# Performance work log

Measured on AMD Instinct MI355X. Metric: run time of the kernel, lower is better.

## Reference

```python
import jax, jax.numpy as jnp
import numpy as np
import math

HIDDEN = 2048
NUM_HEADS = 16
NUM_KV_HEADS = 4
HEAD_DIM = HIDDEN // NUM_HEADS  # 128
INTER = 8192
ROPE_THETA = 10000.0
EPS = 1e-6
B, S = 1, 2048


def _linear_init(key, out_f, in_f):
    return jax.random.normal(key, (out_f, in_f), dtype=jnp.float32) * (2.0 / (in_f + out_f)) ** 0.5


def setup_inputs() -> dict:
    key = jax.random.key(0)
    ks = jax.random.split(key, 10)
    hidden_states = jax.random.normal(ks[0], (B, S, HIDDEN), dtype=jnp.float32)
    # additive causal mask [B, 1, S, S]
    causal = jnp.tril(jnp.ones((S, S), dtype=bool))
    attention_mask = jnp.where(causal, 0.0, -1e9).astype(jnp.float32)[None, None]
    position_ids = jnp.arange(S, dtype=jnp.int32)[None, :]
    return {
        "hidden_states": hidden_states,
        "attention_mask": attention_mask,
        "position_ids": position_ids,
        "norm1_w": jnp.ones((HIDDEN,), dtype=jnp.float32),
        "norm2_w": jnp.ones((HIDDEN,), dtype=jnp.float32),
        "Wq": _linear_init(ks[1], NUM_HEADS * HEAD_DIM, HIDDEN),
        "Wk": _linear_init(ks[2], NUM_KV_HEADS * HEAD_DIM, HIDDEN),
        "Wv": _linear_init(ks[3], NUM_KV_HEADS * HEAD_DIM, HIDDEN),
        "Wo": _linear_init(ks[4], HIDDEN, NUM_HEADS * HEAD_DIM),
        "Wgate": _linear_init(ks[5], INTER, HIDDEN),
        "Wup": _linear_init(ks[6], INTER, HIDDEN),
        "Wdown": _linear_init(ks[7], HIDDEN, INTER),
    }


def _rmsnorm(x, w):
    return x * jax.lax.rsqrt(jnp.mean(x * x, axis=-1, keepdims=True) + EPS) * w


def _apply_rope(x, position_ids):
    # x: [B, H, S, D]; split-half RoPE exactly as the torch module does
    half = x.shape[-1] // 2
    inv_freq = (1.0 / (ROPE_THETA ** (jnp.arange(0, HEAD_DIM, 2, dtype=jnp.float32) / HEAD_DIM)))[:half]
    freqs = jnp.einsum('bi,j->bij', position_ids.astype(jnp.float32), inv_freq)  # [B,S,half]
    cos = jnp.cos(freqs)[:, None]  # [B,1,S,half]
    sin = jnp.sin(freqs)[:, None]
    x1, x2 = x[..., :half], x[..., half:]
    return jnp.concatenate([x1 * cos - x2 * sin, x2 * cos + x1 * sin], axis=-1)


def reference(hidden_states, attention_mask, position_ids, norm1_w, norm2_w,
              Wq, Wk, Wv, Wo, Wgate, Wup, Wdown):
    b, s, _ = hidden_states.shape
    # --- attention sub-block (pre-norm residual) ---
    h = _rmsnorm(hidden_states, norm1_w)
    q = (h @ Wq.T).reshape(b, s, NUM_HEADS, HEAD_DIM).transpose(0, 2, 1, 3)
    k = (h @ Wk.T).reshape(b, s, NUM_KV_HEADS, HEAD_DIM).transpose(0, 2, 1, 3)
    v = (h @ Wv.T).reshape(b, s, NUM_KV_HEADS, HEAD_DIM).transpose(0, 2, 1, 3)
    q = _apply_rope(q, position_ids)
    k = _apply_rope(k, position_ids)
    n_rep = NUM_HEADS // NUM_KV_HEADS
    k = jnp.repeat(k, n_rep, axis=1)  # GQA repeat_interleave over head dim
    v = jnp.repeat(v, n_rep, axis=1)
    scores = jnp.einsum('bhqd,bhkd->bhqk', q, k) / math.sqrt(HEAD_DIM)
    scores = scores + attention_mask
    attn = jax.nn.softmax(scores, axis=-1)
    ctx = jnp.einsum('bhqk,bhkd->bhqd', attn, v).transpose(0, 2, 1, 3).reshape(b, s, -1)
    x = hidden_states + ctx @ Wo.T
    # --- MoE sub-block: num_experts == 1 -> plain SwiGLU MLP ---
    h2 = _rmsnorm(x, norm2_w)
    mlp = (jax.nn.silu(h2 @ Wgate.T) * (h2 @ Wup.T)) @ Wdown.T
    return x + mlp
```

## Files before the change

### kernel.cpp

```cpp
#include <hip/hip_runtime.h>
#include <hip/hip_bf16.h>
#include <math.h>


#define HIDDENC 2048
#define SLEN    2048
#define NHEADS  16
#define NKV     4
#define HD      128
#define INTERC  8192

typedef __attribute__((ext_vector_type(8))) short bf16x8;
typedef __attribute__((ext_vector_type(4))) float f32x4;
typedef __hip_bfloat16 bf16;

__device__ __forceinline__ void gld_lds16(const void* g, void* l) {
    __builtin_amdgcn_global_load_lds((const __attribute__((address_space(1))) void*)g,
                                     (__attribute__((address_space(3))) void*)l, 16, 0, 0);
}

__device__ __forceinline__ unsigned short bf_bits(float x) {
    bf16 t = __float2bfloat16(x);
    return *(unsigned short*)&t;
}
__device__ __forceinline__ float bits_f(short s) {
    bf16 b = *(bf16*)&s;
    return __bfloat162float(b);
}

template <int EPI>
__global__ __launch_bounds__(256) void gemm_bt(const bf16* __restrict__ A,
                                               const bf16* __restrict__ B,
                                               void* __restrict__ Cout,
                                               const float* __restrict__ R,
                                               int M, int N, int K, int lda) {
    constexpr int BM = 128, BN = 128, BK = 64;
    __shared__ bf16 As[BM * BK];
    __shared__ bf16 Bs[BN * BK];
    const int tid  = threadIdx.x;
    const int wave = tid >> 6;
    const int lane = tid & 63;
    const int wm = wave >> 1, wn = wave & 1;
    const long m0 = (long)blockIdx.y * BM;
    const long n0 = (long)blockIdx.x * BN;
    const long kofs = (long)blockIdx.z * K;

    const int srow = wave * 8 + (lane >> 3);
    const int scol = (lane & 7) * 8;
    const bf16* Ag = A + (m0 + srow) * (long)lda + scol + kofs;
    const bf16* Bg = B + (n0 + srow) * (long)lda + scol + kofs;
    bf16* Asw = &As[(wave * 8) * BK];
    bf16* Bsw = &Bs[(wave * 8) * BK];

    f32x4 acc[4][4] = {};
    const int row = lane & 15;
    const int kq  = (lane >> 4) * 8;

    for (int k0 = 0; k0 < K; k0 += BK) {
#pragma unroll
        for (int t = 0; t < 4; t++) {
            gld_lds16(Ag + (long)(t * 32) * lda + k0, Asw + t * 32 * BK);
            gld_lds16(Bg + (long)(t * 32) * lda + k0, Bsw + t * 32 * BK);
        }
        __syncthreads();
#pragma unroll
        for (int kk = 0; kk < BK; kk += 32) {
            bf16x8 af[4], bfr[4];
#pragma unroll
            for (int i = 0; i < 4; i++)
                af[i] = *(const bf16x8*)&As[(wm * 64 + i * 16 + row) * BK + kk + kq];
#pragma unroll
            for (int j = 0; j < 4; j++)
                bfr[j] = *(const bf16x8*)&Bs[(wn * 64 + j * 16 + row) * BK + kk + kq];
#pragma unroll
            for (int i = 0; i < 4; i++)
#pragma unroll
                for (int j = 0; j < 4; j++)
                    acc[i][j] = __builtin_amdgcn_mfma_f32_16x16x32_bf16(af[i], bfr[j], acc[i][j], 0, 0, 0);
        }
        __syncthreads();
    }

    const int quad = lane >> 4;
#pragma unroll
    for (int i = 0; i < 4; i++)
#pragma unroll
        for (int j = 0; j < 4; j++)
#pragma unroll
            for (int r = 0; r < 4; r++) {
                long rr = m0 + wm * 64 + i * 16 + quad * 4 + r;
                long cc = n0 + wn * 64 + j * 16 + (lane & 15);
                float v = acc[i][j][r];
                if (EPI == 0) {
                    ((bf16*)Cout)[rr * N + cc] = __float2bfloat16(v);
                } else if (EPI == 1) {
                    ((float*)Cout)[rr * N + cc] = v + R[rr * N + cc];
                } else {
                    ((float*)Cout)[(long)blockIdx.z * M * N + rr * N + cc] = v;
                }
            }
}

__global__ __launch_bounds__(256) void rmsnorm_kernel(const float* __restrict__ x,
                                                      const float* __restrict__ w,
                                                      bf16* __restrict__ out) {
    const int row = blockIdx.x;
    const int tid = threadIdx.x;
    const float* xr = x + (long)row * HIDDENC;
    float4 a = *(const float4*)&xr[tid * 8];
    float4 b = *(const float4*)&xr[tid * 8 + 4];
    float ss = a.x*a.x + a.y*a.y + a.z*a.z + a.w*a.w + b.x*b.x + b.y*b.y + b.z*b.z + b.w*b.w;
#pragma unroll
    for (int d = 1; d < 64; d <<= 1) ss += __shfl_xor(ss, d, 64);
    __shared__ float wsum[4];
    if ((tid & 63) == 0) wsum[tid >> 6] = ss;
    __syncthreads();
    ss = wsum[0] + wsum[1] + wsum[2] + wsum[3];
    float sc = rsqrtf(ss * (1.0f / HIDDENC) + 1e-6f);
    float4 wa = *(const float4*)&w[tid * 8];
    float4 wb = *(const float4*)&w[tid * 8 + 4];
    float vals[8] = {a.x*wa.x, a.y*wa.y, a.z*wa.z, a.w*wa.w,
                     b.x*wb.x, b.y*wb.y, b.z*wb.z, b.w*wb.w};
    union { bf16x8 v; unsigned short u[8]; } pk;
#pragma unroll
    for (int e = 0; e < 8; e++) pk.u[e] = bf_bits(vals[e] * sc);
    *(bf16x8*)&out[(long)row * HIDDENC + tid * 8] = pk.v;
}

__global__ __launch_bounds__(256) void cvt_kernel(const float* __restrict__ in,
                                                  bf16* __restrict__ out, long n) {
    long idx = ((long)blockIdx.x * 256 + threadIdx.x) * 8;
    if (idx >= n) return;
    float4 a = *(const float4*)&in[idx];
    float4 b = *(const float4*)&in[idx + 4];
    float vals[8] = {a.x, a.y, a.z, a.w, b.x, b.y, b.z, b.w};
    union { bf16x8 v; unsigned short u[8]; } pk;
#pragma unroll
    for (int e = 0; e < 8; e++) pk.u[e] = bf_bits(vals[e]);
    *(bf16x8*)&out[idx] = pk.v;
}

__global__ __launch_bounds__(256) void rope_kernel(bf16* __restrict__ x,
                                                   const int* __restrict__ pos,
                                                   int nheads, int rowstride) {
    long gid = (long)blockIdx.x * 256 + threadIdx.x;
    int i = gid & 63;
    long t = gid >> 6;
    int h = (int)(t % nheads);
    long s = t / nheads;
    if (s >= SLEN) return;
    float inv = __expf(-(float)i * 0.14391156516779195f);
    float f = (float)pos[s] * inv;
    float sn, c;
    sincosf(f, &sn, &c);
    bf16* p = x + s * (long)rowstride + h * HD + i;
    float x1 = __bfloat162float(p[0]);
    float x2 = __bfloat162float(p[64]);
    p[0]  = __float2bfloat16(x1 * c - x2 * sn);
    p[64] = __float2bfloat16(x2 * c + x1 * sn);
}

__global__ __launch_bounds__(256) void flash_attn(const bf16* __restrict__ Q,
                                                  const bf16* __restrict__ Kb,
                                                  const bf16* __restrict__ VT,
                                                  bf16* __restrict__ Ctx) {
    constexpr int QSTR = 2560, PSTR = 68, BKEY = 64;
    __shared__ bf16 Ks[64 * 128];
    __shared__ bf16 Vs[128 * 64];
    __shared__ bf16 Ps[4][16 * PSTR];
    const int qt  = 31 - blockIdx.x;
    const int h   = blockIdx.y;
    const int kvh = h >> 2;
    const int tid = threadIdx.x;
    const int wave = tid >> 6, lane = tid & 63;
    const int quad = lane >> 4, lrow = lane & 15;
    const int qbase = qt * 64 + wave * 16;

    bf16x8 qf[4];
#pragma unroll
    for (int kk = 0; kk < 4; kk++)
        qf[kk] = *(const bf16x8*)&Q[(long)(qbase + lrow) * QSTR + h * HD + kk * 32 + quad * 8];

    f32x4 o[8] = {};
    float mrow[4], lsum[4];
#pragma unroll
    for (int r = 0; r < 4; r++) { mrow[r] = -1e30f; lsum[r] = 0.0f; }

    const int nkt = qt + 1;
    const float scale = 0.08838834764831845f;
    const bf16* Kh  = Kb + kvh * HD;
    const bf16* VTh = VT + (long)(kvh * HD) * SLEN;
    bf16* Pw = Ps[wave];

    for (int kt = 0; kt < nkt; kt++) {
        __syncthreads();
#pragma unroll
        for (int rd = 0; rd < 4; rd++) {
            int id = rd * 256 + tid;
            int row = id >> 4, g = id & 15;
            bf16x8 kv = *(const bf16x8*)&Kh[(long)(kt * BKEY + row) * QSTR + g * 8];
            *(bf16x8*)&Ks[row * 128 + ((g ^ (row & 15)) * 8)] = kv;
        }
#pragma unroll
        for (int rd = 0; rd < 4; rd++) {
            int id = rd * 256 + tid;
            int d = id >> 3, g = id & 7;
            bf16x8 vv = *(const bf16x8*)&VTh[(long)d * SLEN + kt * BKEY + g * 8];
            *(bf16x8*)&Vs[d * 64 + ((g ^ (d & 7)) * 8)] = vv;
        }
        __syncthreads();

        f32x4 sacc[4] = {};
#pragma unroll
        for (int kk = 0; kk < 4; kk++) {
            bf16x8 kb[4];
#pragma unroll
            for (int j = 0; j < 4; j++)
                kb[j] = *(const bf16x8*)&Ks[(j * 16 + lrow) * 128 + (((kk * 4 + quad) ^ lrow) * 8)];
#pragma unroll
            for (int j = 0; j < 4; j++)
                sacc[j] = __builtin_amdgcn_mfma_f32_16x16x32_bf16(qf[kk], kb[j], sacc[j], 0, 0, 0);
        }

        const bool diag = (kt == qt);
#pragma unroll
        for (int j = 0; j < 4; j++)
#pragma unroll
            for (int r = 0; r < 4; r++) {
                float v = sacc[j][r] * scale;
                if (diag) {
                    int rowg = qbase + quad * 4 + r;
                    int colg = qt * 64 + j * 16 + lrow;
                    if (colg > rowg) v = -1e30f;
                }
                sacc[j][r] = v;
            }

        float alpha[4];
#pragma unroll
        for (int r = 0; r < 4; r++) {
            float mx = sacc[0][r];
#pragma unroll
            for (int j = 1; j < 4; j++) mx = fmaxf(mx, sacc[j][r]);
#pragma unroll
            for (int d = 1; d < 16; d <<= 1) mx = fmaxf(mx, __shfl_xor(mx, d, 16));
            float mnew = fmaxf(mrow[r], mx);
            float a = __expf(mrow[r] - mnew);
            mrow[r] = mnew;
            alpha[r] = a;
            float rs = 0.0f;
#pragma unroll
            for (int j = 0; j < 4; j++) {
                float p = __expf(sacc[j][r] - mnew);
                sacc[j][r] = p;
                rs += p;
            }
#pragma unroll
            for (int d = 1; d < 16; d <<= 1) rs += __shfl_xor(rs, d, 16);
            lsum[r] = lsum[r] * a + rs;
        }

#pragma unroll
        for (int dj = 0; dj < 8; dj++)
#pragma unroll
            for (int r = 0; r < 4; r++) o[dj][r] *= alpha[r];

#pragma unroll
        for (int j = 0; j < 4; j++)
#pragma unroll
            for (int r = 0; r < 4; r++)
                Pw[(quad * 4 + r) * PSTR + j * 16 + lrow] = __float2bfloat16(sacc[j][r]);
        __asm__ volatile("s_waitcnt lgkmcnt(0)" ::: "memory");

#pragma unroll
        for (int kk = 0; kk < 2; kk++) {
            bf16x8 pf = *(const bf16x8*)&Pw[lrow * PSTR + kk * 32 + quad * 8];
#pragma unroll
            for (int dj = 0; dj < 8; dj++) {
                int dr = dj * 16 + lrow;
                bf16x8 vb = *(const bf16x8*)&Vs[dr * 64 + (((kk * 4 + quad) ^ (dr & 7)) * 8)];
                o[dj] = __builtin_amdgcn_mfma_f32_16x16x32_bf16(pf, vb, o[dj], 0, 0, 0);
            }
        }
    }

#pragma unroll
    for (int dj = 0; dj < 8; dj++)
#pragma unroll
        for (int r = 0; r < 4; r++) {
            long rowg = qbase + quad * 4 + r;
            long col  = (long)h * HD + dj * 16 + lrow;
            Ctx[rowg * (NHEADS * HD) + col] = __float2bfloat16(o[dj][r] / lsum[r]);
        }
}

__global__ __launch_bounds__(256) void silu_mul_kernel(const bf16* __restrict__ g,
                                                       const bf16* __restrict__ u,
                                                       bf16* __restrict__ out, long n) {
    long idx = ((long)blockIdx.x * 256 + threadIdx.x) * 8;
    if (idx >= n) return;
    bf16x8 gv = *(const bf16x8*)&g[idx];
    bf16x8 uv = *(const bf16x8*)&u[idx];
    union { bf16x8 v; unsigned short w[8]; } pk;
#pragma unroll
    for (int e = 0; e < 8; e++) {
        float gf = bits_f(gv[e]);
        float uf = bits_f(uv[e]);
        float s = gf / (1.0f + __expf(-gf));
        pk.w[e] = bf_bits(s * uf);
    }
    *(bf16x8*)&out[idx] = pk.v;
}

__global__ __launch_bounds__(256) void reduce2_kernel(const float* __restrict__ p,
                                                      float* __restrict__ out, long n) {
    long idx = ((long)blockIdx.x * 256 + threadIdx.x) * 4;
    if (idx >= n) return;
    float4 a = *(const float4*)&p[idx];
    float4 b = *(const float4*)&p[idx + n];
    float4 o = *(const float4*)&out[idx];
    o.x += a.x + b.x; o.y += a.y + b.y; o.z += a.z + b.z; o.w += a.w + b.w;
    *(float4*)&out[idx] = o;
}

extern "C" void kernel_launch(void* const* d_in, const int* in_sizes, int n_in,
                              void* d_out, int out_size, void* d_ws, size_t ws_size,
                              hipStream_t stream) {
    const float* hidden = (const float*)d_in[0];
    const int*   pos    = (const int*)d_in[2];
    const float* n1w    = (const float*)d_in[3];
    const float* n2w    = (const float*)d_in[4];
    const float* Wq     = (const float*)d_in[5];
    const float* Wk     = (const float*)d_in[6];
    const float* Wv     = (const float*)d_in[7];
    const float* Wo     = (const float*)d_in[8];
    const float* Wg     = (const float*)d_in[9];
    const float* Wu     = (const float*)d_in[10];
    const float* Wd     = (const float*)d_in[11];
    float* out = (float*)d_out;

    char* ws = (char*)d_ws;
    const size_t MB = 1ull << 20;
    bf16* h    = (bf16*)(ws + 0);
    bf16* qk   = (bf16*)(ws + 8  * MB);
    bf16* vt   = (bf16*)(ws + 18 * MB);
    bf16* ctx  = (bf16*)(ws + 20 * MB);
    bf16* wqk  = (bf16*)(ws + 28 * MB);
    bf16* wvb  = (bf16*)(ws + 38 * MB);
    bf16*  wg   = (bf16*)(ws + 8   * MB);
    bf16*  wu   = (bf16*)(ws + 40  * MB);
    bf16*  gate = (bf16*)(ws + 72  * MB);
    bf16*  up   = (bf16*)(ws + 104 * MB);
    bf16*  wd   = (bf16*)(ws + 104 * MB);
    float* pbuf = (float*)(ws + 28 * MB);
    bf16* wob = wqk;

    rmsnorm_kernel<<<dim3(2048), dim3(256), 0, stream>>>(hidden, n1w, h);
    cvt_kernel<<<dim3(2048), dim3(256), 0, stream>>>(Wq, wqk,                2048L * 2048);
    cvt_kernel<<<dim3(512),  dim3(256), 0, stream>>>(Wk, wqk + 2048L * 2048, 512L * 2048);
    cvt_kernel<<<dim3(512),  dim3(256), 0, stream>>>(Wv, wvb,                512L * 2048);
    gemm_bt<0><<<dim3(20, 16), dim3(256), 0, stream>>>(h, wqk, qk, nullptr, 2048, 2560, 2048, 2048);
    gemm_bt<0><<<dim3(16, 4),  dim3(256), 0, stream>>>(wvb, h, vt, nullptr, 512, 2048, 2048, 2048);
    rope_kernel<<<dim3(8192), dim3(256), 0, stream>>>(qk, pos, NHEADS, 2560);
    rope_kernel<<<dim3(2048), dim3(256), 0, stream>>>(qk + 2048, pos, NKV, 2560);
    flash_attn<<<dim3(32, 16), dim3(256), 0, stream>>>(qk, qk + 2048, vt, ctx);
    cvt_kernel<<<dim3(2048), dim3(256), 0, stream>>>(Wo, wob, 2048L * 2048);
    gemm_bt<1><<<dim3(16, 16), dim3(256), 0, stream>>>(ctx, wob, out, hidden, 2048, 2048, 2048, 2048);
    rmsnorm_kernel<<<dim3(2048), dim3(256), 0, stream>>>(out, n2w, h);
    cvt_kernel<<<dim3(8192), dim3(256), 0, stream>>>(Wg, wg, 8192L * 2048);
    cvt_kernel<<<dim3(8192), dim3(256), 0, stream>>>(Wu, wu, 8192L * 2048);
    gemm_bt<0><<<dim3(64, 16), dim3(256), 0, stream>>>(h, wg, gate, nullptr, 2048, 8192, 2048, 2048);
    gemm_bt<0><<<dim3(64, 16), dim3(256), 0, stream>>>(h, wu, up,   nullptr, 2048, 8192, 2048, 2048);
    silu_mul_kernel<<<dim3(8192), dim3(256), 0, stream>>>(gate, up, gate, 2048L * 8192);
    cvt_kernel<<<dim3(8192), dim3(256), 0, stream>>>(Wd, wd, 2048L * 8192);
    gemm_bt<2><<<dim3(16, 16, 2), dim3(256), 0, stream>>>(gate, wd, pbuf, nullptr, 2048, 2048, 4096, 8192);
    reduce2_kernel<<<dim3(4096), dim3(256), 0, stream>>>(pbuf, out, 2048L * 2048);
    (void)in_sizes; (void)n_in; (void)out_size; (void)ws_size;
}
```

Baseline: 844.5 us.

## Add 256x256 double-buffered swizzled GEMM for MLP projections with 4-way split-K

Introduces a new 512-thread GEMM kernel with 256x256 tiles, double-buffered LDS staging via direct global-to-LDS loads, XOR-swizzled LDS layout, explicit vmcnt waits and barriers, and MFMA priority raising. It replaces the gate, up and down projections, and the down projection now splits K four ways with a 4-input reduction. The aim is more data reuse per tile and overlap of loads with MFMA work, at the cost of fewer blocks per GEMM and a larger split-K partial buffer.

Result: faster. 758.3 us (-10.2%).

```diff
diff --git a/kernel.cpp b/kernel.cpp
--- a/kernel.cpp
+++ b/kernel.cpp
@@ -27,6 +27,10 @@
     bf16 b = *(bf16*)&s;
     return __bfloat162float(b);
 }
+
+#define SBAR      asm volatile("s_barrier" ::: "memory")
+#define WAIT_VM4  asm volatile("s_waitcnt vmcnt(4)" ::: "memory")
+#define WAIT_VM0  asm volatile("s_waitcnt vmcnt(0)" ::: "memory")
 
 template <int EPI>
 __global__ __launch_bounds__(256) void gemm_bt(const bf16* __restrict__ A,
@@ -43,12 +47,11 @@
     const int wm = wave >> 1, wn = wave & 1;
     const long m0 = (long)blockIdx.y * BM;
     const long n0 = (long)blockIdx.x * BN;
-    const long kofs = (long)blockIdx.z * K;
 
     const int srow = wave * 8 + (lane >> 3);
     const int scol = (lane & 7) * 8;
-    const bf16* Ag = A + (m0 + srow) * (long)lda + scol + kofs;
-    const bf16* Bg = B + (n0 + srow) * (long)lda + scol + kofs;
+    const bf16* Ag = A + (m0 + srow) * (long)lda + scol;
+    const bf16* Bg = B + (n0 + srow) * (long)lda + scol;
     bf16* Asw = &As[(wave * 8) * BK];
     bf16* Bsw = &Bs[(wave * 8) * BK];
 
@@ -93,8 +96,122 @@
                 float v = acc[i][j][r];
                 if (EPI == 0) {
                     ((bf16*)Cout)[rr * N + cc] = __float2bfloat16(v);
-                } else if (EPI == 1) {
+                } else {
                     ((float*)Cout)[rr * N + cc] = v + R[rr * N + cc];
+                }
+            }
+}
+
+template <int EPI>
+__global__ __launch_bounds__(512) void gemm256(const bf16* __restrict__ A,
+                                               const bf16* __restrict__ B,
+                                               void* __restrict__ Cout,
+                                               int M, int N, int K, int lda) {
+    __shared__ __align__(16) bf16 smem[2][2][256 * 64];
+    const int tid  = threadIdx.x;
+    const int wave = tid >> 6, lane = tid & 63;
+    const int wm = wave >> 2, wn = wave & 3;
+    const int quad = lane >> 4, lrow = lane & 15;
+    const long m0 = (long)blockIdx.y * 256;
+    const long n0 = (long)blockIdx.x * 256;
+    const long kofs = (long)blockIdx.z * K;
+
+    const int srow  = tid >> 3;
+    const int gphys = tid & 7;
+    const int glog  = gphys ^ (srow & 7);
+    const bf16* Ag = A + (m0 + srow) * (long)lda + kofs + glog * 8;
+    const bf16* Bg = B + (n0 + srow) * (long)lda + kofs + glog * 8;
+
+    auto stageA = [&](int tt) {
+#pragma unroll
+        for (int rr = 0; rr < 4; rr++)
+            gld_lds16(Ag + ((long)tt << 6) + (long)(rr * 64) * lda,
+                      &smem[tt & 1][0][tid * 8 + rr * 4096]);
+    };
+    auto stageB = [&](int tt, int hh) {
+#pragma unroll
+        for (int r2 = 0; r2 < 2; r2++) {
+            int rr = hh * 2 + r2;
+            gld_lds16(Bg + ((long)tt << 6) + (long)(rr * 64) * lda,
+                      &smem[tt & 1][1][tid * 8 + rr * 4096]);
+        }
+    };
+
+    f32x4 acc[8][4] = {};
+    const int swz = (quad ^ (lrow & 7)) * 8;
+    const int NT = K >> 6;
+
+    stageA(0);
+    stageB(0, 0); stageB(0, 1);
+    if (NT > 1) { stageB(1, 0); stageB(1, 1); }
+    WAIT_VM4;
+    SBAR;
+
+    for (int t = 0; t < NT; ++t) {
+        const bf16* smA = &smem[t & 1][0][0];
+        const bf16* smB = &smem[t & 1][1][0];
+        bf16x8 bq[4][2], aq[2][2];
+
+#pragma unroll
+        for (int n = 0; n < 4; n++)
+#pragma unroll
+            for (int ks = 0; ks < 2; ks++)
+                bq[n][ks] = *(const bf16x8*)&smB[(wn * 64 + n * 16 + lrow) * 64 + (swz ^ (ks * 32))];
+#pragma unroll
+        for (int i = 0; i < 2; i++)
+#pragma unroll
+            for (int ks = 0; ks < 2; ks++)
+                aq[i][ks] = *(const bf16x8*)&smA[(wm * 128 + i * 16 + lrow) * 64 + (swz ^ (ks * 32))];
+        if (t + 1 < NT) stageA(t + 1);
+        SBAR;
+        __builtin_amdgcn_s_setprio(1);
+#pragma unroll
+        for (int i = 0; i < 2; i++)
+#pragma unroll
+            for (int n = 0; n < 4; n++) {
+                acc[i][n] = __builtin_amdgcn_mfma_f32_16x16x32_bf16(aq[i][0], bq[n][0], acc[i][n], 0, 0, 0);
+                acc[i][n] = __builtin_amdgcn_mfma_f32_16x16x32_bf16(aq[i][1], bq[n][1], acc[i][n], 0, 0, 0);
+            }
+        __builtin_amdgcn_s_setprio(0);
+        SBAR;
+
+#pragma unroll
+        for (int q = 1; q < 4; q++) {
+#pragma unroll
+            for (int i = 0; i < 2; i++)
+#pragma unroll
+                for (int ks = 0; ks < 2; ks++)
+                    aq[i][ks] = *(const bf16x8*)&smA[(wm * 128 + (q * 2 + i) * 16 + lrow) * 64 + (swz ^ (ks * 32))];
+            if (q == 1) { if (t + 2 < NT) stageB(t + 2, 0); }
+            if (q == 2) { if (t + 2 < NT) stageB(t + 2, 1); }
+            SBAR;
+            __builtin_amdgcn_s_setprio(1);
+#pragma unroll
+            for (int i = 0; i < 2; i++)
+#pragma unroll
+                for (int n = 0; n < 4; n++) {
+                    acc[q * 2 + i][n] = __builtin_amdgcn_mfma_f32_16x16x32_bf16(aq[i][0], bq[n][0], acc[q * 2 + i][n], 0, 0, 0);
+                    acc[q * 2 + i][n] = __builtin_amdgcn_mfma_f32_16x16x32_bf16(aq[i][1], bq[n][1], acc[q * 2 + i][n], 0, 0, 0);
+                }
+            __builtin_amdgcn_s_setprio(0);
+            if (q == 3) {
+                if (t + 2 < NT) { WAIT_VM4; } else { WAIT_VM0; }
+            }
+            SBAR;
+        }
+    }
+
+#pragma unroll
+    for (int i = 0; i < 8; i++)
+#pragma unroll
+        for (int n = 0; n < 4; n++)
+#pragma unroll
+            for (int r = 0; r < 4; r++) {
+                long rr = m0 + wm * 128 + i * 16 + quad * 4 + r;
+                long cc = n0 + wn * 64 + n * 16 + lrow;
+                float v = acc[i][n][r];
+                if (EPI == 0) {
+                    ((bf16*)Cout)[rr * N + cc] = __float2bfloat16(v);
                 } else {
                     ((float*)Cout)[(long)blockIdx.z * M * N + rr * N + cc] = v;
                 }
@@ -312,14 +429,19 @@
     *(bf16x8*)&out[idx] = pk.v;
 }
 
-__global__ __launch_bounds__(256) void reduce2_kernel(const float* __restrict__ p,
+__global__ __launch_bounds__(256) void reduce4_kernel(const float* __restrict__ p,
                                                       float* __restrict__ out, long n) {
     long idx = ((long)blockIdx.x * 256 + threadIdx.x) * 4;
     if (idx >= n) return;
     float4 a = *(const float4*)&p[idx];
     float4 b = *(const float4*)&p[idx + n];
+    float4 c = *(const float4*)&p[idx + 2 * n];
+    float4 d = *(const float4*)&p[idx + 3 * n];
     float4 o = *(const float4*)&out[idx];
-    o.x += a.x + b.x; o.y += a.y + b.y; o.z += a.z + b.z; o.w += a.w + b.w;
+    o.x += a.x + b.x + c.x + d.x;
+    o.y += a.y + b.y + c.y + d.y;
+    o.z += a.z + b.z + c.z + d.z;
+    o.w += a.w + b.w + c.w + d.w;
     *(float4*)&out[idx] = o;
 }
 
@@ -352,7 +474,7 @@
     bf16*  gate = (bf16*)(ws + 72  * MB);
     bf16*  up   = (bf16*)(ws + 104 * MB);
     bf16*  wd   = (bf16*)(ws + 104 * MB);
-    float* pbuf = (float*)(ws + 28 * MB);
+    float* pbuf = (float*)(ws + 0);
     bf16* wob = wqk;
 
     rmsnorm_kernel<<<dim3(2048), dim3(256), 0, stream>>>(hidden, n1w, h);
@@ -369,11 +491,11 @@
     rmsnorm_kernel<<<dim3(2048), dim3(256), 0, stream>>>(out, n2w, h);
     cvt_kernel<<<dim3(8192), dim3(256), 0, stream>>>(Wg, wg, 8192L * 2048);
     cvt_kernel<<<dim3(8192), dim3(256), 0, stream>>>(Wu, wu, 8192L * 2048);
-    gemm_bt<0><<<dim3(64, 16), dim3(256), 0, stream>>>(h, wg, gate, nullptr, 2048, 8192, 2048, 2048);
-    gemm_bt<0><<<dim3(64, 16), dim3(256), 0, stream>>>(h, wu, up,   nullptr, 2048, 8192, 2048, 2048);
+    gemm256<0><<<dim3(32, 8), dim3(512), 0, stream>>>(h, wg, gate, 2048, 8192, 2048, 2048);
+    gemm256<0><<<dim3(32, 8), dim3(512), 0, stream>>>(h, wu, up,   2048, 8192, 2048, 2048);
     silu_mul_kernel<<<dim3(8192), dim3(256), 0, stream>>>(gate, up, gate, 2048L * 8192);
     cvt_kernel<<<dim3(8192), dim3(256), 0, stream>>>(Wd, wd, 2048L * 8192);
-    gemm_bt<2><<<dim3(16, 16, 2), dim3(256), 0, stream>>>(gate, wd, pbuf, nullptr, 2048, 2048, 4096, 8192);
-    reduce2_kernel<<<dim3(4096), dim3(256), 0, stream>>>(pbuf, out, 2048L * 2048);
+    gemm256<2><<<dim3(8, 8, 4), dim3(512), 0, stream>>>(gate, wd, pbuf, 2048, 2048, 2048, 8192);
+    reduce4_kernel<<<dim3(4096), dim3(256), 0, stream>>>(pbuf, out, 2048L * 2048);
     (void)in_sizes; (void)n_in; (void)out_size; (void)ws_size;
 }
```
